# Performance work log

Measured on AMD Instinct MI355X. Metric: run time of the kernel, lower is better.

Reference implementation:

```python
import jax, jax.numpy as jnp
import numpy as np

B, S, D = 2, 2048, 4096
H, KV, HD = 32, 8, 128          # n_heads, n_kv_heads, head_dim
N_REP = H // KV                  # GQA repeat factor
THETA = 500000.0


def setup_inputs() -> dict:
    key = jax.random.key(0)
    ks = jax.random.split(key, 5)
    x = jax.random.normal(ks[0], (B, S, D), jnp.float32)
    wq = jax.random.normal(ks[1], (D, H * HD), jnp.float32) * (D ** -0.5)
    wk = jax.random.normal(ks[2], (D, KV * HD), jnp.float32) * (D ** -0.5)
    wv = jax.random.normal(ks[3], (D, KV * HD), jnp.float32) * (D ** -0.5)
    wo = jax.random.normal(ks[4], (H * HD, D), jnp.float32) * ((H * HD) ** -0.5)
    # precomputed rotary frequencies (cos/sin of freqs_cis = exp(i * pos * inv_freq))
    inv_freq = 1.0 / (THETA ** (jnp.arange(0, HD, 2, dtype=jnp.float32) / HD))
    ang = jnp.arange(S, dtype=jnp.float32)[:, None] * inv_freq[None, :]  # [S, HD/2]
    freqs_cos = jnp.cos(ang)
    freqs_sin = jnp.sin(ang)
    # causal additive mask (prefill, start_pos=0)
    mask = jnp.triu(jnp.full((S, S), -1e9, jnp.float32), k=1)
    return dict(x=x, freqs_cos=freqs_cos, freqs_sin=freqs_sin, mask=mask,
                wq=wq, wk=wk, wv=wv, wo=wo, start_pos=0)


def _rope(t, cos, sin):
    # t: [B, S, nh, HD]; complex-pair rotation on interleaved (even, odd) channels
    tr = t.reshape(*t.shape[:-1], HD // 2, 2)
    te, to = tr[..., 0], tr[..., 1]
    c = cos[None, :, None, :]
    s = sin[None, :, None, :]
    out = jnp.stack([te * c - to * s, te * s + to * c], axis=-1)
    return out.reshape(t.shape)


def reference(x, freqs_cos, freqs_sin, mask, wq, wk, wv, wo, start_pos):
    q = (x @ wq).reshape(B, S, H, HD)
    k = (x @ wk).reshape(B, S, KV, HD)
    v = (x @ wv).reshape(B, S, KV, HD)
    q = _rope(q, freqs_cos, freqs_sin)
    k = _rope(k, freqs_cos, freqs_sin)
    # prefill: cache[:, :start_pos+S] == (k, v) since start_pos == 0
    # GQA: group query heads over KV heads instead of materializing repeat_kv
    qg = q.reshape(B, S, KV, N_REP, HD)
    scores = jnp.einsum('bqgrd,bkgd->bgrqk', qg, k) / jnp.sqrt(jnp.float32(HD))
    scores = scores + mask  # broadcast [S,S] additive causal mask
    probs = jax.nn.softmax(scores.astype(jnp.float32), axis=-1).astype(q.dtype)
    out = jnp.einsum('bgrqk,bkgd->bqgrd', probs, v).reshape(B, S, H * HD)
    return out @ wo
```

## Files before the change

kernel.cpp:

```cpp
#include <hip/hip_runtime.h>

typedef unsigned short u16;
typedef unsigned int u32;

typedef __bf16 bf16x8 __attribute__((ext_vector_type(8)));
typedef float f32x4 __attribute__((ext_vector_type(4)));

#define SEQ 2048
#define NH 32
#define NKV 8
#define HDIM 128
#define KB 32
#define QKVW 6144
#define KCOL 4096
#define VCOL 5120

__device__ __forceinline__ float b2f(u16 u) {
    return __uint_as_float(((u32)u) << 16);
}
__device__ __forceinline__ u16 f2bf(float f) {
    u32 u = __float_as_uint(f);
    u += 0x7fff + ((u >> 16) & 1);
    return (u16)(u >> 16);
}

#define GLDS16(g, l)                                                            \
    __builtin_amdgcn_global_load_lds(                                           \
        (const __attribute__((address_space(1))) void*)(g),                     \
        (__attribute__((address_space(3))) void*)(l), 16, 0, 0)

__global__ __launch_bounds__(1024) void transcvt_k(const float* __restrict__ in,
                                                   u16* __restrict__ out,
                                                   int K, int N) {
    __shared__ float tile[32][33];
    int n0 = blockIdx.x * 32, k0 = blockIdx.y * 32;
    tile[threadIdx.y][threadIdx.x] = in[(size_t)(k0 + threadIdx.y) * N + n0 + threadIdx.x];
    __syncthreads();
    out[(size_t)(n0 + threadIdx.y) * K + k0 + threadIdx.x] = f2bf(tile[threadIdx.x][threadIdx.y]);
}

__global__ __launch_bounds__(256) void cvt_k(const float* __restrict__ in,
                                             u16* __restrict__ out) {
    size_t i = ((size_t)blockIdx.x * 256 + threadIdx.x) * 8;
    float4 f0 = *(const float4*)(in + i);
    float4 f1 = *(const float4*)(in + i + 4);
    union { uint4 u4; u16 h[8]; } pk;
    pk.h[0] = f2bf(f0.x); pk.h[1] = f2bf(f0.y);
    pk.h[2] = f2bf(f0.z); pk.h[3] = f2bf(f0.w);
    pk.h[4] = f2bf(f1.x); pk.h[5] = f2bf(f1.y);
    pk.h[6] = f2bf(f1.z); pk.h[7] = f2bf(f1.w);
    *(uint4*)(out + i) = pk.u4;
}

template <bool OUT_F32>
__global__ __launch_bounds__(256) void gemm128(const u16* __restrict__ A,
                                               const u16* __restrict__ BT,
                                               void* __restrict__ Cv,
                                               int M, int N, int K) {
    __shared__ __align__(16) u16 As[128 * 32];
    __shared__ __align__(16) u16 Bs[128 * 32];
    const int t = threadIdx.x, lane = t & 63, w = t >> 6;
    const int m0 = blockIdx.y * 128, n0 = blockIdx.x * 128;
    const int wm = (w & 1) * 64, wn = (w >> 1) * 64;
    const int row16 = lane & 15, q8 = (lane >> 4) * 8;
    f32x4 acc[4][4] = {};

    const size_t arow = (size_t)(m0 + w * 32 + (lane >> 2)) * K + (lane & 3) * 8;
    const size_t brow = (size_t)(n0 + w * 32 + (lane >> 2)) * K + (lane & 3) * 8;
    char* asb = (char*)As + w * 2048;
    char* bsb = (char*)Bs + w * 2048;

    for (int kt = 0; kt < K; kt += 32) {
        GLDS16(A + arow + kt, asb);
        GLDS16(A + arow + (size_t)16 * K + kt, asb + 1024);
        GLDS16(BT + brow + kt, bsb);
        GLDS16(BT + brow + (size_t)16 * K + kt, bsb + 1024);
        __syncthreads();
        bf16x8 af[4], bf[4];
        for (int mi = 0; mi < 4; ++mi)
            af[mi] = *(const bf16x8*)&As[(wm + mi * 16 + row16) * 32 + q8];
        for (int ni = 0; ni < 4; ++ni)
            bf[ni] = *(const bf16x8*)&Bs[(wn + ni * 16 + row16) * 32 + q8];
        for (int mi = 0; mi < 4; ++mi)
            for (int ni = 0; ni < 4; ++ni)
                acc[mi][ni] = __builtin_amdgcn_mfma_f32_16x16x32_bf16(af[mi], bf[ni], acc[mi][ni], 0, 0, 0);
        __syncthreads();
    }

    const int r0 = (lane >> 4) * 4;
    for (int mi = 0; mi < 4; ++mi) {
        for (int r = 0; r < 4; ++r) {
            size_t row = (size_t)(m0 + wm + mi * 16 + r0 + r) * N + n0 + wn;
            for (int ni = 0; ni < 4; ++ni) {
                if constexpr (OUT_F32)
                    ((float*)Cv)[row + ni * 16 + row16] = acc[mi][ni][r];
                else
                    ((u16*)Cv)[row + ni * 16 + row16] = f2bf(acc[mi][ni][r]);
            }
        }
    }
}

__global__ __launch_bounds__(256) void rope_k(u16* __restrict__ T, int col0,
                                              const float* __restrict__ cosb,
                                              const float* __restrict__ sinb,
                                              int nh) {
    int i = blockIdx.x * 256 + threadIdx.x;
    int p = i & 63;
    int h = (i >> 6) % nh;
    int bs = i / (64 * nh);
    int s = bs & (SEQ - 1);
    size_t base = (size_t)bs * QKVW + col0 + h * HDIM + 2 * p;
    ushort2 v = *(ushort2*)(T + base);
    float te = b2f(v.x), to = b2f(v.y);
    float c = cosb[s * 64 + p], sn = sinb[s * 64 + p];
    ushort2 o;
    o.x = f2bf(te * c - to * sn);
    o.y = f2bf(te * sn + to * c);
    *(ushort2*)(T + base) = o;
}

__global__ __launch_bounds__(1024) void vtrans_k(const u16* __restrict__ QKV,
                                                 u16* __restrict__ VtG) {
    __shared__ u16 tile[32][33];
    int s0 = blockIdx.x * 32, d0 = blockIdx.y * 32, plane = blockIdx.z;
    int b = plane >> 3, g = plane & 7;
    tile[threadIdx.y][threadIdx.x] =
        QKV[(size_t)(b * SEQ + s0 + threadIdx.y) * QKVW + VCOL + g * HDIM + d0 + threadIdx.x];
    __syncthreads();
    VtG[((size_t)plane * HDIM + d0 + threadIdx.y) * SEQ + s0 + threadIdx.x] =
        tile[threadIdx.x][threadIdx.y];
}

__global__ __launch_bounds__(256) void fattn_k(const u16* __restrict__ QKV,
                                               const u16* __restrict__ VtG,
                                               u16* __restrict__ O) {
    __shared__ __align__(16) u16 Ks[KB][136];
    __shared__ __align__(16) u16 Vt[HDIM][40];
    __shared__ __align__(16) u16 Ps[4][16][40];

    const int q0 = (gridDim.x - 1 - blockIdx.x) * 64;
    const int h = blockIdx.y, b = blockIdx.z;
    const int g = h >> 2;
    const int t = threadIdx.x, lane = t & 63, w = t >> 6;
    const int row16 = lane & 15, q8 = (lane >> 4) * 8, q84 = (lane >> 4) * 4;
    const float scale = 0.08838834764831845f;

    bf16x8 qf[4];
    {
        const u16* qptr = QKV + (size_t)(b * SEQ + q0 + w * 16 + row16) * QKVW + h * HDIM;
        for (int c = 0; c < 4; ++c) qf[c] = *(const bf16x8*)(qptr + c * 32 + q8);
    }

    f32x4 o[8];
    for (int c = 0; c < 8; ++c) o[c] = (f32x4){0.f, 0.f, 0.f, 0.f};
    float lsum[4] = {0.f, 0.f, 0.f, 0.f};

    const u16* kbase = QKV + (size_t)b * SEQ * QKVW + KCOL + g * HDIM;
    const u16* vtp = VtG + (size_t)(b * NKV + g) * HDIM * SEQ;

    const int ntiles = (q0 + 63) / KB + 1;
    for (int tile = 0; tile < ntiles; ++tile) {
        const int jb = tile * KB;
        __syncthreads();
        for (int i = 0; i < 2; ++i) {
            int c = t + 256 * i;
            int kr = c >> 4, kc = (c & 15) * 8;
            *(uint4*)&Ks[kr][kc] = *(const uint4*)(kbase + (size_t)(jb + kr) * QKVW + kc);
            int vr = c >> 2, vc = (c & 3) * 8;
            *(uint4*)&Vt[vr][vc] = *(const uint4*)(vtp + (size_t)vr * SEQ + jb + vc);
        }
        __syncthreads();

        for (int sub = 0; sub < 2; ++sub) {
            f32x4 sa = {0.f, 0.f, 0.f, 0.f};
            for (int c = 0; c < 4; ++c) {
                bf16x8 kf = *(const bf16x8*)&Ks[sub * 16 + row16][c * 32 + q8];
                sa = __builtin_amdgcn_mfma_f32_16x16x32_bf16(qf[c], kf, sa, 0, 0, 0);
            }
            const int kcol = jb + sub * 16 + row16;
            for (int r = 0; r < 4; ++r) {
                int qrow = q0 + w * 16 + q84 + r;
                float p = (kcol <= qrow) ? __expf(fminf(sa[r] * scale, 80.f)) : 0.f;
                lsum[r] += p;
                Ps[w][q84 + r][sub * 16 + row16] = f2bf(p);
            }
        }
        bf16x8 pf = *(const bf16x8*)&Ps[w][row16][q8];
        for (int c = 0; c < 8; ++c) {
            bf16x8 vf = *(const bf16x8*)&Vt[c * 16 + row16][q8];
            o[c] = __builtin_amdgcn_mfma_f32_16x16x32_bf16(pf, vf, o[c], 0, 0, 0);
        }
    }

    for (int r = 0; r < 4; ++r)
        for (int off = 1; off < 16; off <<= 1) lsum[r] += __shfl_xor(lsum[r], off);

    float inv[4];
    for (int r = 0; r < 4; ++r) inv[r] = 1.f / lsum[r];

    u16* optr = O + (size_t)(b * SEQ + q0 + w * 16) * (NH * HDIM) + h * HDIM;
    for (int c = 0; c < 8; ++c)
        for (int r = 0; r < 4; ++r)
            optr[(size_t)(q84 + r) * (NH * HDIM) + c * 16 + row16] = f2bf(o[c][r] * inv[r]);
}

extern "C" void kernel_launch(void* const* d_in, const int* in_sizes, int n_in,
                              void* d_out, int out_size, void* d_ws, size_t ws_size,
                              hipStream_t stream) {
    const float* x    = (const float*)d_in[0];
    const float* fcos = (const float*)d_in[1];
    const float* fsin = (const float*)d_in[2];
    const float* wq = (const float*)d_in[4];
    const float* wk = (const float*)d_in[5];
    const float* wv = (const float*)d_in[6];
    const float* wo = (const float*)d_in[7];
    float* out = (float*)d_out;

    char* wsp = (char*)d_ws;
    u16* BTall = (u16*)(wsp);
    u16* VtG   = (u16*)(wsp);
    u16* woT   = (u16*)(wsp + 50331648);
    u16* xb    = (u16*)(wsp + 83886080);
    u16* ATb   = (u16*)(wsp + 83886080);
    u16* QKVb  = (u16*)(wsp + 117440512);

    const int M = 2 * SEQ;
    const int D = 4096;
    const int NQ = NH * HDIM;

    dim3 tb(32, 32);
    transcvt_k<<<dim3(4096 / 32, D / 32), tb, 0, stream>>>(wq, BTall, D, 4096);
    transcvt_k<<<dim3(1024 / 32, D / 32), tb, 0, stream>>>(wk, BTall + (size_t)4096 * 4096, D, 1024);
    transcvt_k<<<dim3(1024 / 32, D / 32), tb, 0, stream>>>(wv, BTall + (size_t)5120 * 4096, D, 1024);
    transcvt_k<<<dim3(D / 32, NQ / 32), tb, 0, stream>>>(wo, woT, NQ, D);
    cvt_k<<<(M * D) / (256 * 8), 256, 0, stream>>>(x, xb);

    gemm128<false><<<dim3(QKVW / 128, M / 128), 256, 0, stream>>>(xb, BTall, QKVb, M, QKVW, D);

    rope_k<<<(M * NH * 64) / 256, 256, 0, stream>>>(QKVb, 0, fcos, fsin, NH);
    rope_k<<<(M * NKV * 64) / 256, 256, 0, stream>>>(QKVb, KCOL, fcos, fsin, NKV);

    vtrans_k<<<dim3(SEQ / 32, HDIM / 32, 2 * NKV), tb, 0, stream>>>(QKVb, VtG);

    fattn_k<<<dim3(SEQ / 64, NH, 2), 256, 0, stream>>>(QKVb, VtG, ATb);

    gemm128<true><<<dim3(D / 128, M / 128), 256, 0, stream>>>(ATb, woT, out, M, D, NQ);

    (void)in_sizes; (void)n_in; (void)out_size; (void)ws_size;
}
```

Before: 1.004 ms.

## Replace 128x128 GEMM with 256x256 double-buffered, swizzled, phase-pipelined GEMM

Replaces the simple 128x128 tile GEMM, which synchronizes twice per K-step, with a 256x256 tile, 512-thread kernel. It uses a 128KB double-buffered LDS, XOR-swizzled LDS layout, BK=64, and four interleaved load/MFMA phases with setprio and explicit waitcnt so global-to-LDS copies overlap with compute. The goal is better data reuse per tile and hiding memory latency in both the QKV and output projection GEMMs. In exchange it uses far more LDS and registers and launches fewer blocks: QKV gets 24x16 blocks and the output projection 16x16, which may leave CUs underused on a large-CU GPU.

```diff
diff --git a/kernel.cpp b/kernel.cpp
--- a/kernel.cpp
+++ b/kernel.cpp
@@ -53,49 +53,149 @@
 }
 
 template <bool OUT_F32>
-__global__ __launch_bounds__(256) void gemm128(const u16* __restrict__ A,
-                                               const u16* __restrict__ BT,
-                                               void* __restrict__ Cv,
-                                               int M, int N, int K) {
-    __shared__ __align__(16) u16 As[128 * 32];
-    __shared__ __align__(16) u16 Bs[128 * 32];
+__global__ __launch_bounds__(512, 2) void gemm256(const u16* __restrict__ A,
+                                                  const u16* __restrict__ BT,
+                                                  void* __restrict__ Cv,
+                                                  int M, int N, int K) {
+    __shared__ __align__(16) char L[131072];
     const int t = threadIdx.x, lane = t & 63, w = t >> 6;
-    const int m0 = blockIdx.y * 128, n0 = blockIdx.x * 128;
-    const int wm = (w & 1) * 64, wn = (w >> 1) * 64;
-    const int row16 = lane & 15, q8 = (lane >> 4) * 8;
-    f32x4 acc[4][4] = {};
-
-    const size_t arow = (size_t)(m0 + w * 32 + (lane >> 2)) * K + (lane & 3) * 8;
-    const size_t brow = (size_t)(n0 + w * 32 + (lane >> 2)) * K + (lane & 3) * 8;
-    char* asb = (char*)As + w * 2048;
-    char* bsb = (char*)Bs + w * 2048;
-
-    for (int kt = 0; kt < K; kt += 32) {
-        GLDS16(A + arow + kt, asb);
-        GLDS16(A + arow + (size_t)16 * K + kt, asb + 1024);
-        GLDS16(BT + brow + kt, bsb);
-        GLDS16(BT + brow + (size_t)16 * K + kt, bsb + 1024);
-        __syncthreads();
-        bf16x8 af[4], bf[4];
+    const int wr = w >> 2, wc = w & 3;
+    const int m0 = blockIdx.y * 256, n0 = blockIdx.x * 256;
+    const int r16 = lane & 15;
+    const int woff = w * 1024;
+    const int w8l = w * 8 + (lane >> 3);
+    const int cswz = ((lane & 7) ^ (lane >> 3)) * 8;
+    const u16* sA = A + (size_t)(m0 + w8l) * K + cswz;
+    const u16* sB = BT + (size_t)(n0 + w8l) * K + cswz;
+
+    const int acol0 = ((lane >> 4) * 16) ^ ((lane & 7) << 4);
+    const int acol1 = (((lane >> 4) * 16) + 64) ^ ((lane & 7) << 4);
+    const char* arowp = L + (wr * 128 + r16) * 128;
+    const char* browp = L + 32768 + (wc * 64 + r16) * 128;
+
+    f32x4 acc[8][4] = {};
+    bf16x8 a[4][2], b0[2][2], b1[2][2];
+
+    auto stage = [&](int bufi, int isB, int h, int kt) {
+        const u16* s = isB ? sB : sA;
+        char* d = (char*)L + bufi * 65536 + isB * 32768 + h * 16384 + woff;
+        GLDS16(s + (size_t)(h * 128) * K + kt, d);
+        GLDS16(s + (size_t)(h * 128 + 64) * K + kt, d + 8192);
+    };
+
+    const int NT = K >> 6;
+    stage(0, 0, 0, 0); stage(0, 0, 1, 0); stage(0, 1, 0, 0); stage(0, 1, 1, 0);
+    if (NT > 1) {
+        stage(1, 0, 0, 64);
+        asm volatile("s_waitcnt vmcnt(2)" ::: "memory");
+    } else {
+        asm volatile("s_waitcnt vmcnt(0)" ::: "memory");
+    }
+    __builtin_amdgcn_s_barrier();
+    __builtin_amdgcn_sched_barrier(0);
+
+    for (int T = 0; T < NT; ++T) {
+        const int buf = T & 1;
+        const char* Ab = arowp + buf * 65536;
+        const char* Bb = browp + buf * 65536;
+        const int ktn = (T + 1) << 6, ktn2 = (T + 2) << 6;
+
+#pragma unroll
+        for (int mi = 0; mi < 4; ++mi) {
+            a[mi][0] = *(const bf16x8*)(Ab + mi * 2048 + acol0);
+            a[mi][1] = *(const bf16x8*)(Ab + mi * 2048 + acol1);
+        }
+#pragma unroll
+        for (int ni = 0; ni < 2; ++ni) {
+            b0[ni][0] = *(const bf16x8*)(Bb + ni * 2048 + acol0);
+            b0[ni][1] = *(const bf16x8*)(Bb + ni * 2048 + acol1);
+        }
+        if (T + 1 < NT) stage(buf ^ 1, 0, 1, ktn);
+        __builtin_amdgcn_s_barrier();
+        __builtin_amdgcn_sched_barrier(0);
+        asm volatile("s_waitcnt lgkmcnt(0)" ::: "memory");
+        __builtin_amdgcn_s_setprio(1);
+#pragma unroll
         for (int mi = 0; mi < 4; ++mi)
-            af[mi] = *(const bf16x8*)&As[(wm + mi * 16 + row16) * 32 + q8];
-        for (int ni = 0; ni < 4; ++ni)
-            bf[ni] = *(const bf16x8*)&Bs[(wn + ni * 16 + row16) * 32 + q8];
+#pragma unroll
+            for (int ni = 0; ni < 2; ++ni) {
+                acc[mi][ni] = __builtin_amdgcn_mfma_f32_16x16x32_bf16(a[mi][0], b0[ni][0], acc[mi][ni], 0, 0, 0);
+                acc[mi][ni] = __builtin_amdgcn_mfma_f32_16x16x32_bf16(a[mi][1], b0[ni][1], acc[mi][ni], 0, 0, 0);
+            }
+        __builtin_amdgcn_s_setprio(0);
+        __builtin_amdgcn_s_barrier();
+        __builtin_amdgcn_sched_barrier(0);
+
+#pragma unroll
+        for (int ni = 0; ni < 2; ++ni) {
+            b1[ni][0] = *(const bf16x8*)(Bb + (ni + 2) * 2048 + acol0);
+            b1[ni][1] = *(const bf16x8*)(Bb + (ni + 2) * 2048 + acol1);
+        }
+        if (T + 1 < NT) stage(buf ^ 1, 1, 0, ktn);
+        __builtin_amdgcn_s_barrier();
+        __builtin_amdgcn_sched_barrier(0);
+        asm volatile("s_waitcnt lgkmcnt(0)" ::: "memory");
+        __builtin_amdgcn_s_setprio(1);
+#pragma unroll
         for (int mi = 0; mi < 4; ++mi)
-            for (int ni = 0; ni < 4; ++ni)
-                acc[mi][ni] = __builtin_amdgcn_mfma_f32_16x16x32_bf16(af[mi], bf[ni], acc[mi][ni], 0, 0, 0);
-        __syncthreads();
+#pragma unroll
+            for (int ni = 0; ni < 2; ++ni) {
+                acc[mi][ni + 2] = __builtin_amdgcn_mfma_f32_16x16x32_bf16(a[mi][0], b1[ni][0], acc[mi][ni + 2], 0, 0, 0);
+                acc[mi][ni + 2] = __builtin_amdgcn_mfma_f32_16x16x32_bf16(a[mi][1], b1[ni][1], acc[mi][ni + 2], 0, 0, 0);
+            }
+        __builtin_amdgcn_s_setprio(0);
+        __builtin_amdgcn_s_barrier();
+        __builtin_amdgcn_sched_barrier(0);
+
+#pragma unroll
+        for (int mi = 0; mi < 4; ++mi) {
+            a[mi][0] = *(const bf16x8*)(Ab + (mi + 4) * 2048 + acol0);
+            a[mi][1] = *(const bf16x8*)(Ab + (mi + 4) * 2048 + acol1);
+        }
+        if (T + 1 < NT) stage(buf ^ 1, 1, 1, ktn);
+        __builtin_amdgcn_s_barrier();
+        __builtin_amdgcn_sched_barrier(0);
+        asm volatile("s_waitcnt lgkmcnt(0)" ::: "memory");
+        __builtin_amdgcn_s_setprio(1);
+#pragma unroll
+        for (int mi = 0; mi < 4; ++mi)
+#pragma unroll
+            for (int ni = 0; ni < 2; ++ni) {
+                acc[mi + 4][ni] = __builtin_amdgcn_mfma_f32_16x16x32_bf16(a[mi][0], b0[ni][0], acc[mi + 4][ni], 0, 0, 0);
+                acc[mi + 4][ni] = __builtin_amdgcn_mfma_f32_16x16x32_bf16(a[mi][1], b0[ni][1], acc[mi + 4][ni], 0, 0, 0);
+            }
+        __builtin_amdgcn_s_setprio(0);
+        __builtin_amdgcn_s_barrier();
+        __builtin_amdgcn_sched_barrier(0);
+
+        if (T + 2 < NT) stage(buf, 0, 0, ktn2);
+        __builtin_amdgcn_s_setprio(1);
+#pragma unroll
+        for (int mi = 0; mi < 4; ++mi)
+#pragma unroll
+            for (int ni = 0; ni < 2; ++ni) {
+                acc[mi + 4][ni + 2] = __builtin_amdgcn_mfma_f32_16x16x32_bf16(a[mi][0], b1[ni][0], acc[mi + 4][ni + 2], 0, 0, 0);
+                acc[mi + 4][ni + 2] = __builtin_amdgcn_mfma_f32_16x16x32_bf16(a[mi][1], b1[ni][1], acc[mi + 4][ni + 2], 0, 0, 0);
+            }
+        __builtin_amdgcn_s_setprio(0);
+        if (T + 2 < NT) asm volatile("s_waitcnt vmcnt(2)" ::: "memory");
+        else            asm volatile("s_waitcnt vmcnt(0)" ::: "memory");
+        __builtin_amdgcn_s_barrier();
+        __builtin_amdgcn_sched_barrier(0);
     }
 
     const int r0 = (lane >> 4) * 4;
-    for (int mi = 0; mi < 4; ++mi) {
+#pragma unroll
+    for (int mi = 0; mi < 8; ++mi) {
+#pragma unroll
         for (int r = 0; r < 4; ++r) {
-            size_t row = (size_t)(m0 + wm + mi * 16 + r0 + r) * N + n0 + wn;
+            size_t row = (size_t)(m0 + wr * 128 + mi * 16 + r0 + r) * N + n0 + wc * 64;
+#pragma unroll
             for (int ni = 0; ni < 4; ++ni) {
                 if constexpr (OUT_F32)
-                    ((float*)Cv)[row + ni * 16 + row16] = acc[mi][ni][r];
+                    ((float*)Cv)[row + ni * 16 + r16] = acc[mi][ni][r];
                 else
-                    ((u16*)Cv)[row + ni * 16 + row16] = f2bf(acc[mi][ni][r]);
+                    ((u16*)Cv)[row + ni * 16 + r16] = f2bf(acc[mi][ni][r]);
             }
         }
     }
@@ -236,7 +336,7 @@
     transcvt_k<<<dim3(D / 32, NQ / 32), tb, 0, stream>>>(wo, woT, NQ, D);
     cvt_k<<<(M * D) / (256 * 8), 256, 0, stream>>>(x, xb);
 
-    gemm128<false><<<dim3(QKVW / 128, M / 128), 256, 0, stream>>>(xb, BTall, QKVb, M, QKVW, D);
+    gemm256<false><<<dim3(QKVW / 256, M / 256), 512, 0, stream>>>(xb, BTall, QKVb, M, QKVW, D);
 
     rope_k<<<(M * NH * 64) / 256, 256, 0, stream>>>(QKVb, 0, fcos, fsin, NH);
     rope_k<<<(M * NKV * 64) / 256, 256, 0, stream>>>(QKVb, KCOL, fcos, fsin, NKV);
@@ -245,7 +345,7 @@
 
     fattn_k<<<dim3(SEQ / 64, NH, 2), 256, 0, stream>>>(QKVb, VtG, ATb);
 
-    gemm128<true><<<dim3(D / 128, M / 128), 256, 0, stream>>>(ATb, woT, out, M, D, NQ);
+    gemm256<true><<<dim3(D / 256, M / 256), 512, 0, stream>>>(ATb, woT, out, M, D, NQ);
 
     (void)in_sizes; (void)n_in; (void)out_size; (void)ws_size;
 }
```

Result: faster. 884.3 us (-11.9%).
